# Optimization experiments

Hardware: AMD Instinct MI355X
Metric: run time of the kernel (lower is better)

Reference implementation:

```python
import jax, jax.numpy as jnp
import numpy as np

B, H, W, D = 16, 64, 64, 512

def setup_inputs() -> dict:
    key = jax.random.key(0)
    k1, k2, k3, k4, k5, k6 = jax.random.split(key, 6)
    x = jax.random.normal(k1, (B, H, W, D), dtype=jnp.float32)
    attentionXFull = jax.random.normal(k2, (B, H, W, W), dtype=jnp.float32)
    attentionYFull = jax.random.normal(k3, (B, W, H, H), dtype=jnp.float32)
    valueFull = jax.random.normal(k4, (B, H, W, D), dtype=jnp.float32)
    # Learned scalar Gaussian params: shift initialized positive, bias negative
    shift = jnp.abs(jax.random.normal(k5, (1,), dtype=jnp.float32))
    bias = -jnp.abs(jax.random.normal(k6, (1,), dtype=jnp.float32))
    return {"x": x, "attentionXFull": attentionXFull, "attentionYFull": attentionYFull,
            "valueFull": valueFull, "shift": shift, "bias": bias}

def reference(x, attentionXFull, attentionYFull, valueFull, shift, bias):
    # valueFull: [B,H,W,D]; attentionXFull: [B,H,W,W] (last axis = row positions h)
    # attentionYFull: [B,W,H,H] (indexed [b,c,r,w], last axis = col positions w)
    Bv, Hd, Wd, Dd = valueFull.shape
    cw = jnp.arange(Wd, dtype=valueFull.dtype)
    # disX[c,h] = -(shift*(h-c)^2 + bias)
    disX = -(shift[0] * (cw[None, :] - cw[:, None]) ** 2 + bias[0])  # [W,W]
    aX = jax.nn.sigmoid(disX[None, None, :, :] + attentionXFull)     # [B,H,W,W]
    outX = jnp.einsum('brch,brhd->brcd', aX, valueFull)              # row attention
    rh = jnp.arange(Hd, dtype=valueFull.dtype)
    # disY[r,w] = -(shift*(w-r)^2 + bias)
    disY = -(shift[0] * (rh[None, :] - rh[:, None]) ** 2 + bias[0])  # [H,H]
    aY = jax.nn.sigmoid(disY[None, None, :, :] + attentionYFull)     # [B,W,H,H] as [b,c,r,w]
    outY = jnp.einsum('bcrw,bwcd->brcd', aY, valueFull)              # column attention
    return outX + outY
```

## Files before the change

### kernel.cpp

```cpp
#include <hip/hip_runtime.h>
#include <stdint.h>


typedef __attribute__((ext_vector_type(8))) __bf16 bf16x8;
typedef __attribute__((ext_vector_type(8))) short short8;
typedef __attribute__((ext_vector_type(4))) float f32x4;
typedef __attribute__((ext_vector_type(4))) unsigned int uint4v;

union U8 { short8 s; bf16x8 b; unsigned short u[8]; uint4v q; };

__device__ __forceinline__ unsigned short f2bf(float f) {
    union { float f; unsigned int i; } v; v.f = f;
    return (unsigned short)((v.i + 0x7fffu + ((v.i >> 16) & 1u)) >> 16);
}
__device__ __forceinline__ float fsigmoid(float x) {
    float e = __builtin_amdgcn_exp2f(-1.44269504f * x);
    return __builtin_amdgcn_rcpf(1.0f + e);
}

template <int S_I, int S_K, bool ACCUM>
__global__ __launch_bounds__(256)
void gauss_gemm(const float* __restrict__ att,
                const float* __restrict__ V,
                float* __restrict__ out,
                const float* __restrict__ shiftp,
                const float* __restrict__ biasp) {
    __shared__ unsigned short S[4096];
    __shared__ unsigned short VT[128 * 66];

    const int bid    = blockIdx.x;
    const int dq     = bid & 3;
    const int i      = (bid >> 2) & 63;
    const int b      = bid >> 8;
    const int t      = threadIdx.x;
    const int dstart = dq * 128;

    const float shift = shiftp[0];
    const float bias  = biasp[0];

    const size_t base = (size_t)b * 2097152 + (size_t)i * S_I;

    const float* ab = att + (size_t)(b * 64 + i) * 4096;
#pragma unroll
    for (int chunk = 0; chunk < 2; ++chunk) {
        int flat = t + chunk * 256;
        int q = flat >> 6, m = flat & 63;
        const float* ap = ab + m * 64 + q * 8;
        f32x4 av0 = *(const f32x4*)(ap);
        f32x4 av1 = *(const f32x4*)(ap + 4);
        U8 res;
#pragma unroll
        for (int j = 0; j < 8; ++j) {
            float a    = (j < 4) ? av0[j & 3] : av1[j & 3];
            float diff = (float)(q * 8 + j - m);
            float dis  = -(shift * diff * diff + bias);
            res.u[j]   = f2bf(fsigmoid(dis + a));
        }
        *(short8*)(&S[flat * 8]) = res.s;
    }

    {
        const float* vb = V + base + dstart;
        const int d4 = t & 31;
        const int h0 = t >> 5;
#pragma unroll
        for (int it = 0; it < 8; ++it) {
            const int h = h0 + it * 8;
            f32x4 v = *(const f32x4*)(vb + (size_t)h * S_K + 4 * d4);
#pragma unroll
            for (int u = 0; u < 4; ++u)
                VT[(4 * d4 + u) * 66 + h] = f2bf(v[u]);
        }
    }
    __syncthreads();

    const int lane = t & 63, wid = t >> 6;
    const int l15 = lane & 15, quad = lane >> 4;

    f32x4 acc[4][2];
#pragma unroll
    for (int mt = 0; mt < 4; ++mt)
#pragma unroll
        for (int nt = 0; nt < 2; ++nt) acc[mt][nt] = (f32x4)0.0f;

#pragma unroll
    for (int ks = 0; ks < 2; ++ks) {
        bf16x8 af[4];
#pragma unroll
        for (int mt = 0; mt < 4; ++mt) {
            U8 a;
            a.s = *(const short8*)(&S[((ks * 4 + quad) * 64 + mt * 16 + l15) * 8]);
            af[mt] = a.b;
        }
        const int h = ks * 32 + quad * 8;
#pragma unroll
        for (int nt = 0; nt < 2; ++nt) {
            const int dloc = wid * 32 + nt * 16 + l15;
            const unsigned short* vp = &VT[dloc * 66 + h];
            U8 bvec;
            uint4v qv;
#pragma unroll
            for (int u = 0; u < 4; ++u) qv[u] = *(const unsigned int*)(vp + 2 * u);
            bvec.q = qv;
#pragma unroll
            for (int mt = 0; mt < 4; ++mt)
                acc[mt][nt] = __builtin_amdgcn_mfma_f32_16x16x32_bf16(
                    af[mt], bvec.b, acc[mt][nt], 0, 0, 0);
        }
    }

    float* ob = out + base + dstart;
#pragma unroll
    for (int mt = 0; mt < 4; ++mt)
#pragma unroll
        for (int nt = 0; nt < 2; ++nt)
#pragma unroll
            for (int reg = 0; reg < 4; ++reg) {
                int m = mt * 16 + quad * 4 + reg;
                int d = wid * 32 + nt * 16 + l15;
                size_t off = (size_t)m * S_K + d;
                float v = acc[mt][nt][reg];
                if (ACCUM) v += ob[off];
                ob[off] = v;
            }
}

extern "C" void kernel_launch(void* const* d_in, const int* in_sizes, int n_in,
                              void* d_out, int out_size, void* d_ws, size_t ws_size,
                              hipStream_t stream) {
    const float* attX = (const float*)d_in[1];
    const float* attY = (const float*)d_in[2];
    const float* V    = (const float*)d_in[3];
    const float* shp  = (const float*)d_in[4];
    const float* bip  = (const float*)d_in[5];
    float* out = (float*)d_out;

    dim3 blk(256);
    dim3 grid(16 * 64 * 4);
    gauss_gemm<32768, 512, false><<<grid, blk, 0, stream>>>(attX, V, out, shp, bip);
    gauss_gemm<512, 32768, true><<<grid, blk, 0, stream>>>(attY, V, out, shp, bip);
}
```

Measured before the change: 414.6 us.

## Precompute bf16 sigmoid attention and fuse row/column attention into one kernel

A new prep kernel computes the Gaussian-biased sigmoid for both attention tensors once and stores them as bf16 in the workspace. A fused kernel then computes row and column attention for a (batch, row-half, d-slice) tile. It keeps the row result in LDS as fp16 and adds it to the column result before a single write, which removes the output read-modify-write and the second pass over V. The risks are an extra round trip of the attention tensors through the workspace, fp16 rounding of the intermediate, and heavy LDS and register use. The old two-kernel path remains as a fallback when the workspace is too small.

```diff
diff --git a/kernel.cpp b/kernel.cpp
--- a/kernel.cpp
+++ b/kernel.cpp
@@ -6,6 +6,7 @@
 typedef __attribute__((ext_vector_type(8))) short short8;
 typedef __attribute__((ext_vector_type(4))) float f32x4;
 typedef __attribute__((ext_vector_type(4))) unsigned int uint4v;
+typedef __attribute__((ext_vector_type(4))) unsigned short u16x4;
 
 union U8 { short8 s; bf16x8 b; unsigned short u[8]; uint4v q; };
 
@@ -16,6 +17,192 @@
 __device__ __forceinline__ float fsigmoid(float x) {
     float e = __builtin_amdgcn_exp2f(-1.44269504f * x);
     return __builtin_amdgcn_rcpf(1.0f + e);
+}
+__device__ __forceinline__ unsigned short f2h(float f) {
+    union { _Float16 h; unsigned short u; } v; v.h = (_Float16)f; return v.u;
+}
+__device__ __forceinline__ float h2f(unsigned short u) {
+    union { _Float16 h; unsigned short us; } v; v.us = u; return (float)v.h;
+}
+
+__device__ __forceinline__ int sx_addr(int r, int d, int h) {
+    return r * 1024 + d * 64 + (h & 7) + ((((h >> 3) ^ (d & 7))) << 3);
+}
+__device__ __forceinline__ int sy_addr(int c, int d, int w) {
+    return c * 512 + d * 32 + (w & 7) + (((w >> 3) ^ (d & 3) ^ ((c & 1) << 1)) << 3);
+}
+__device__ __forceinline__ int ol_addr(int d, int r, int c) {
+    return d * 2048 + r * 64 + (c ^ ((r & 3) << 2) ^ ((d >> 2) << 4));
+}
+
+__device__ __forceinline__ void sig16(const float* __restrict__ in,
+                                      unsigned short* __restrict__ outp,
+                                      int l0, int sec, float shift, float bias) {
+    f32x4 v[4];
+#pragma unroll
+    for (int j = 0; j < 4; ++j) v[j] = *(const f32x4*)(in + 4 * j);
+    U8 r0, r1;
+#pragma unroll
+    for (int e = 0; e < 16; ++e) {
+        float dd = (float)(l0 + e - sec);
+        float dis = -(shift * dd * dd + bias);
+        unsigned short us = f2bf(fsigmoid(dis + v[e >> 2][e & 3]));
+        if (e < 8) r0.u[e] = us; else r1.u[e - 8] = us;
+    }
+    *(uint4v*)(outp) = r0.q;
+    *(uint4v*)(outp + 8) = r1.q;
+}
+
+__global__ __launch_bounds__(256)
+void prep_sig(const float* __restrict__ attX, const float* __restrict__ attY,
+              unsigned short* __restrict__ aX, unsigned short* __restrict__ aY,
+              const float* __restrict__ shiftp, const float* __restrict__ biasp) {
+    const float shift = shiftp[0];
+    const float bias  = biasp[0];
+    const size_t base = ((size_t)blockIdx.x * 256 + threadIdx.x) * 16;
+    const int sec = (int)((base >> 6) & 63);
+    const int l0  = (int)(base & 63);
+    sig16(attX + base, aX + base, l0, sec, shift, bias);
+    sig16(attY + base, aY + base, l0, sec, shift, bias);
+}
+
+__global__ __launch_bounds__(512, 2)
+void gauss_fused(const unsigned short* __restrict__ aX,
+                 const unsigned short* __restrict__ aY,
+                 const float* __restrict__ V,
+                 float* __restrict__ out) {
+    __shared__ unsigned short slab[32768];
+    __shared__ unsigned short olds[32768];
+
+    const int p   = blockIdx.x;
+    const int xcd = p & 7;
+    const int k   = p >> 3;
+    const int b   = ((k >> 5) << 3) | xcd;
+    const int dg  = (k & 31) >> 1;
+    const int rh  = k & 1;
+    const int rbase = rh * 32;
+
+    const int t    = threadIdx.x;
+    const int lane = t & 63;
+    const int wid  = t >> 6;
+    const int cg   = wid & 3;
+    const int rg   = wid >> 2;
+    const int l15  = lane & 15;
+    const int quad = lane >> 4;
+
+    const size_t vbase = (size_t)b * 2097152;
+
+#pragma unroll
+    for (int dc = 0; dc < 2; ++dc) {
+        const int dstart = dg * 32 + dc * 16;
+
+        __syncthreads();
+
+        {
+            const int r  = t >> 4;
+            const int hq = t & 15;
+            const float* vp = V + vbase + (size_t)(rbase + r) * 32768
+                            + (size_t)(4 * hq) * 512 + dstart;
+            f32x4 vv[4][4];
+#pragma unroll
+            for (int i = 0; i < 4; ++i)
+#pragma unroll
+                for (int j = 0; j < 4; ++j)
+                    vv[i][j] = *(const f32x4*)(vp + i * 512 + 4 * j);
+#pragma unroll
+            for (int d = 0; d < 16; ++d) {
+                u16x4 pk;
+#pragma unroll
+                for (int i = 0; i < 4; ++i) pk[i] = f2bf(vv[i][d >> 2][d & 3]);
+                *(u16x4*)&slab[sx_addr(r, d, 4 * hq)] = pk;
+            }
+        }
+        __syncthreads();
+
+        f32x4 accX[16];
+#pragma unroll
+        for (int rr = 0; rr < 16; ++rr) accX[rr] = (f32x4)0.0f;
+#pragma unroll
+        for (int ks = 0; ks < 2; ++ks) {
+            bf16x8 af[16];
+#pragma unroll
+            for (int rr = 0; rr < 16; ++rr) {
+                const unsigned short* ap = aX
+                    + ((size_t)((b * 64 + rbase + rg * 16 + rr) * 64 + (cg * 16 + l15))) * 64
+                    + ks * 32 + quad * 8;
+                U8 u; u.q = *(const uint4v*)ap; af[rr] = u.b;
+            }
+#pragma unroll
+            for (int rr = 0; rr < 16; ++rr) {
+                U8 bu;
+                bu.q = *(const uint4v*)&slab[sx_addr(rg * 16 + rr, l15, ks * 32 + quad * 8)];
+                accX[rr] = __builtin_amdgcn_mfma_f32_16x16x32_bf16(af[rr], bu.b, accX[rr], 0, 0, 0);
+            }
+        }
+
+#pragma unroll
+        for (int rr = 0; rr < 16; ++rr) {
+            u16x4 pk;
+#pragma unroll
+            for (int reg = 0; reg < 4; ++reg) pk[reg] = f2h(accX[rr][reg]);
+            *(u16x4*)&olds[ol_addr(l15, rg * 16 + rr, cg * 16 + quad * 4)] = pk;
+        }
+
+        f32x4 accY[16];
+#pragma unroll
+        for (int cc = 0; cc < 16; ++cc) accY[cc] = (f32x4)0.0f;
+#pragma unroll
+        for (int half = 0; half < 2; ++half) {
+            __syncthreads();
+            {
+                const int c  = t >> 3;
+                const int wq = t & 7;
+                const float* vp = V + vbase + (size_t)(half * 32 + 4 * wq) * 32768
+                                + (size_t)c * 512 + dstart;
+                f32x4 vv[4][4];
+#pragma unroll
+                for (int i = 0; i < 4; ++i)
+#pragma unroll
+                    for (int j = 0; j < 4; ++j)
+                        vv[i][j] = *(const f32x4*)(vp + (size_t)i * 32768 + 4 * j);
+#pragma unroll
+                for (int d = 0; d < 16; ++d) {
+                    u16x4 pk;
+#pragma unroll
+                    for (int i = 0; i < 4; ++i) pk[i] = f2bf(vv[i][d >> 2][d & 3]);
+                    *(u16x4*)&slab[sy_addr(c, d, 4 * wq)] = pk;
+                }
+            }
+            __syncthreads();
+            bf16x8 bg[16];
+#pragma unroll
+            for (int cc = 0; cc < 16; ++cc) {
+                const unsigned short* ap = aY
+                    + ((size_t)((b * 64 + cg * 16 + cc) * 64 + (rbase + rg * 16 + l15))) * 64
+                    + half * 32 + quad * 8;
+                U8 u; u.q = *(const uint4v*)ap; bg[cc] = u.b;
+            }
+#pragma unroll
+            for (int cc = 0; cc < 16; ++cc) {
+                U8 au;
+                au.q = *(const uint4v*)&slab[sy_addr(cg * 16 + cc, l15, quad * 8)];
+                accY[cc] = __builtin_amdgcn_mfma_f32_16x16x32_bf16(au.b, bg[cc], accY[cc], 0, 0, 0);
+            }
+        }
+
+        {
+            float* ob = out + vbase + (size_t)(rbase + rg * 16 + l15) * 32768 + dstart + quad * 4;
+#pragma unroll
+            for (int cc = 0; cc < 16; ++cc) {
+                f32x4 res;
+#pragma unroll
+                for (int reg = 0; reg < 4; ++reg)
+                    res[reg] = accY[cc][reg]
+                             + h2f(olds[ol_addr(quad * 4 + reg, rg * 16 + l15, cg * 16 + cc)]);
+                *(f32x4*)(ob + (size_t)(cg * 16 + cc) * 512) = res;
+            }
+        }
+    }
 }
 
 template <int S_I, int S_K, bool ACCUM>
@@ -37,7 +224,6 @@
 
     const float shift = shiftp[0];
     const float bias  = biasp[0];
-
     const size_t base = (size_t)b * 2097152 + (size_t)i * S_I;
 
     const float* ab = att + (size_t)(b * 64 + i) * 4096;
@@ -58,7 +244,6 @@
         }
         *(short8*)(&S[flat * 8]) = res.s;
     }
-
     {
         const float* vb = V + base + dstart;
         const int d4 = t & 31;
@@ -135,8 +320,16 @@
     const float* bip  = (const float*)d_in[5];
     float* out = (float*)d_out;
 
-    dim3 blk(256);
-    dim3 grid(16 * 64 * 4);
-    gauss_gemm<32768, 512, false><<<grid, blk, 0, stream>>>(attX, V, out, shp, bip);
-    gauss_gemm<512, 32768, true><<<grid, blk, 0, stream>>>(attY, V, out, shp, bip);
-}
+    const size_t ATT_ELEMS = 16ull * 64 * 64 * 64;
+    if (ws_size >= ATT_ELEMS * 2 * sizeof(unsigned short)) {
+        unsigned short* aXw = (unsigned short*)d_ws;
+        unsigned short* aYw = aXw + ATT_ELEMS;
+        prep_sig<<<dim3(1024), dim3(256), 0, stream>>>(attX, attY, aXw, aYw, shp, bip);
+        gauss_fused<<<dim3(512), dim3(512), 0, stream>>>(aXw, aYw, V, out);
+    } else {
+        dim3 blk(256);
+        dim3 grid(16 * 64 * 4);
+        gauss_gemm<32768, 512, false><<<grid, blk, 0, stream>>>(attX, V, out, shp, bip);
+        gauss_gemm<512, 32768, true><<<grid, blk, 0, stream>>>(attY, V, out, shp, bip);
+    }
+}
```

After: 474.8 us. 1.15x slower.

## Precompute bf16 sigmoid weights and retiled V, fuse row and column attention

Applied to the files above, without the earlier changes.

Adds a prep kernel that computes both Gaussian-biased sigmoid attention maps into bf16 workspace buffers. Two retile kernels also write transposed bf16 copies of V for the row and column directions. A single single-wave MFMA kernel then computes the row result, holds it in LDS as fp16, adds the column result and writes the output once. This removes the read-modify-write of the output between two passes. In exchange it adds extra workspace traffic for the retiled V copies and loses some precision by keeping the row partial in fp16. The old path is kept as a fallback when the workspace is too small.

```diff
diff --git a/kernel.cpp b/kernel.cpp
--- a/kernel.cpp
+++ b/kernel.cpp
@@ -6,6 +6,7 @@
 typedef __attribute__((ext_vector_type(8))) short short8;
 typedef __attribute__((ext_vector_type(4))) float f32x4;
 typedef __attribute__((ext_vector_type(4))) unsigned int uint4v;
+typedef __attribute__((ext_vector_type(4))) unsigned short u16x4;
 
 union U8 { short8 s; bf16x8 b; unsigned short u[8]; uint4v q; };
 
@@ -16,6 +17,142 @@
 __device__ __forceinline__ float fsigmoid(float x) {
     float e = __builtin_amdgcn_exp2f(-1.44269504f * x);
     return __builtin_amdgcn_rcpf(1.0f + e);
+}
+__device__ __forceinline__ unsigned short f2h(float f) {
+    union { _Float16 h; unsigned short u; } v; v.h = (_Float16)f; return v.u;
+}
+__device__ __forceinline__ float h2f(unsigned short u) {
+    union { _Float16 h; unsigned short us; } v; v.us = u; return (float)v.h;
+}
+
+__device__ __forceinline__ void sig16(const float* __restrict__ in,
+                                      unsigned short* __restrict__ outp,
+                                      int l0, int sec, float shift, float bias) {
+    f32x4 v[4];
+#pragma unroll
+    for (int j = 0; j < 4; ++j) v[j] = *(const f32x4*)(in + 4 * j);
+    U8 r0, r1;
+#pragma unroll
+    for (int e = 0; e < 16; ++e) {
+        float dd = (float)(l0 + e - sec);
+        float dis = -(shift * dd * dd + bias);
+        unsigned short us = f2bf(fsigmoid(dis + v[e >> 2][e & 3]));
+        if (e < 8) r0.u[e] = us; else r1.u[e - 8] = us;
+    }
+    *(uint4v*)(outp) = r0.q;
+    *(uint4v*)(outp + 8) = r1.q;
+}
+
+__global__ __launch_bounds__(256)
+void prep_sig(const float* __restrict__ attX, const float* __restrict__ attY,
+              unsigned short* __restrict__ aX, unsigned short* __restrict__ aY,
+              const float* __restrict__ shiftp, const float* __restrict__ biasp) {
+    const float shift = shiftp[0];
+    const float bias  = biasp[0];
+    const size_t base = ((size_t)blockIdx.x * 256 + threadIdx.x) * 16;
+    const int sec = (int)((base >> 6) & 63);
+    const int l0  = (int)(base & 63);
+    sig16(attX + base, aX + base, l0, sec, shift, bias);
+    sig16(attY + base, aY + base, l0, sec, shift, bias);
+}
+
+__global__ __launch_bounds__(256)
+void retile(const float* __restrict__ V, unsigned short* __restrict__ vt,
+            long long rowStride, long long strideB, long long strideI) {
+    __shared__ unsigned short T[64 * 72];
+    const int p = blockIdx.x;
+    const int t = threadIdx.x;
+    const float* src = V + (size_t)(p >> 6) * strideB + (size_t)(p & 63) * strideI;
+    unsigned short* dst = vt + (size_t)p * 32768;
+
+    for (int ch = 0; ch < 8; ++ch) {
+        const int j = t >> 2, qq = t & 3;
+        const float* sp = src + (size_t)j * rowStride + ch * 64 + qq * 16;
+        f32x4 x[4];
+#pragma unroll
+        for (int k = 0; k < 4; ++k) x[k] = *(const f32x4*)(sp + 4 * k);
+        if (ch) __syncthreads();
+        U8 w0, w1;
+#pragma unroll
+        for (int e = 0; e < 8; ++e) {
+            w0.u[e] = f2bf(x[e >> 2][e & 3]);
+            w1.u[e] = f2bf(x[2 + (e >> 2)][e & 3]);
+        }
+        *(uint4v*)(&T[j * 72 + qq * 16])     = w0.q;
+        *(uint4v*)(&T[j * 72 + qq * 16 + 8]) = w1.q;
+        __syncthreads();
+        const int d = t >> 2, part = t & 3;
+        U8 o0, o1;
+#pragma unroll
+        for (int jj = 0; jj < 8; ++jj) {
+            o0.u[jj] = T[(part * 16 + jj) * 72 + d];
+            o1.u[jj] = T[(part * 16 + 8 + jj) * 72 + d];
+        }
+        unsigned short* dp = dst + (size_t)(ch * 64 + d) * 64 + part * 16;
+        *(uint4v*)dp       = o0.q;
+        *(uint4v*)(dp + 8) = o1.q;
+    }
+}
+
+__global__ __launch_bounds__(64, 4)
+void gauss_mfma(const unsigned short* __restrict__ aX,
+                const unsigned short* __restrict__ aY,
+                const unsigned short* __restrict__ vtX,
+                const unsigned short* __restrict__ vtY,
+                float* __restrict__ out) {
+    __shared__ unsigned short olds[16 * 264 + 8];
+
+    const int p  = blockIdx.x;
+    const int b  = (p & 7) + (((p >> 3) >> 9) << 3);
+    const int q  = (p >> 3) & 511;
+    const int dt = q >> 4;
+    const int rt = (q >> 2) & 3;
+    const int ct = q & 3;
+
+    const int lane = threadIdx.x;
+    const int l15 = lane & 15, quad = lane >> 4;
+    const int dlo = dt * 16 + l15;
+
+#pragma unroll
+    for (int rr = 0; rr < 16; ++rr) {
+        const int r = rt * 16 + rr;
+        const unsigned short* vp = vtX + ((size_t)(b * 64 + r) * 512 + dlo) * 64 + quad * 8;
+        const unsigned short* ap = aX + ((size_t)(b * 64 + r) * 64 + ct * 16 + l15) * 64 + quad * 8;
+        U8 v0, v1, a0, a1;
+        v0.q = *(const uint4v*)vp;
+        v1.q = *(const uint4v*)(vp + 32);
+        a0.q = *(const uint4v*)ap;
+        a1.q = *(const uint4v*)(ap + 32);
+        f32x4 acc = (f32x4)0.0f;
+        acc = __builtin_amdgcn_mfma_f32_16x16x32_bf16(v0.b, a0.b, acc, 0, 0, 0);
+        acc = __builtin_amdgcn_mfma_f32_16x16x32_bf16(v1.b, a1.b, acc, 0, 0, 0);
+        u16x4 pk;
+#pragma unroll
+        for (int g = 0; g < 4; ++g) pk[g] = f2h(acc[g]);
+        *(u16x4*)&olds[rr * 264 + l15 * 16 + quad * 4] = pk;
+    }
+
+    float* ob = out + (size_t)b * 2097152 + (size_t)(rt * 16 + l15) * 32768
+              + (size_t)(ct * 16) * 512 + dt * 16 + quad * 4;
+#pragma unroll
+    for (int cc = 0; cc < 16; ++cc) {
+        const int c = ct * 16 + cc;
+        const unsigned short* wp = vtY + ((size_t)(b * 64 + c) * 512 + dlo) * 64 + quad * 8;
+        const unsigned short* bp = aY + ((size_t)(b * 64 + c) * 64 + rt * 16 + l15) * 64 + quad * 8;
+        U8 w0, w1, y0, y1;
+        w0.q = *(const uint4v*)wp;
+        w1.q = *(const uint4v*)(wp + 32);
+        y0.q = *(const uint4v*)bp;
+        y1.q = *(const uint4v*)(bp + 32);
+        f32x4 acc = (f32x4)0.0f;
+        acc = __builtin_amdgcn_mfma_f32_16x16x32_bf16(w0.b, y0.b, acc, 0, 0, 0);
+        acc = __builtin_amdgcn_mfma_f32_16x16x32_bf16(w1.b, y1.b, acc, 0, 0, 0);
+        u16x4 xp = *(const u16x4*)&olds[l15 * 264 + cc * 16 + quad * 4];
+        f32x4 res;
+#pragma unroll
+        for (int g = 0; g < 4; ++g) res[g] = acc[g] + h2f(xp[g]);
+        *(f32x4*)(ob + (size_t)cc * 512) = res;
+    }
 }
 
 template <int S_I, int S_K, bool ACCUM>
@@ -37,28 +174,26 @@
 
     const float shift = shiftp[0];
     const float bias  = biasp[0];
-
     const size_t base = (size_t)b * 2097152 + (size_t)i * S_I;
 
     const float* ab = att + (size_t)(b * 64 + i) * 4096;
 #pragma unroll
     for (int chunk = 0; chunk < 2; ++chunk) {
         int flat = t + chunk * 256;
-        int q = flat >> 6, m = flat & 63;
-        const float* ap = ab + m * 64 + q * 8;
+        int qd = flat >> 6, m = flat & 63;
+        const float* ap = ab + m * 64 + qd * 8;
         f32x4 av0 = *(const f32x4*)(ap);
         f32x4 av1 = *(const f32x4*)(ap + 4);
         U8 res;
 #pragma unroll
         for (int j = 0; j < 8; ++j) {
             float a    = (j < 4) ? av0[j & 3] : av1[j & 3];
-            float diff = (float)(q * 8 + j - m);
+            float diff = (float)(qd * 8 + j - m);
             float dis  = -(shift * diff * diff + bias);
             res.u[j]   = f2bf(fsigmoid(dis + a));
         }
         *(short8*)(&S[flat * 8]) = res.s;
     }
-
     {
         const float* vb = V + base + dstart;
         const int d4 = t & 31;
@@ -135,8 +270,23 @@
     const float* bip  = (const float*)d_in[5];
     float* out = (float*)d_out;
 
-    dim3 blk(256);
-    dim3 grid(16 * 64 * 4);
-    gauss_gemm<32768, 512, false><<<grid, blk, 0, stream>>>(attX, V, out, shp, bip);
-    gauss_gemm<512, 32768, true><<<grid, blk, 0, stream>>>(attY, V, out, shp, bip);
-}
+    const size_t A_ELEMS  = 4194304;
+    const size_t VT_ELEMS = 33554432;
+    const size_t NEED = (2 * A_ELEMS + 2 * VT_ELEMS) * sizeof(unsigned short);
+
+    if (ws_size >= NEED) {
+        unsigned short* aXw = (unsigned short*)d_ws;
+        unsigned short* aYw = aXw + A_ELEMS;
+        unsigned short* vtX = aYw + A_ELEMS;
+        unsigned short* vtY = vtX + VT_ELEMS;
+        prep_sig<<<dim3(1024), dim3(256), 0, stream>>>(attX, attY, aXw, aYw, shp, bip);
+        retile<<<dim3(1024), dim3(256), 0, stream>>>(V, vtX, 512LL, 2097152LL, 32768LL);
+        retile<<<dim3(1024), dim3(256), 0, stream>>>(V, vtY, 32768LL, 2097152LL, 512LL);
+        gauss_mfma<<<dim3(8192), dim3(64), 0, stream>>>(aXw, aYw, vtX, vtY, out);
+    } else {
+        dim3 blk(256);
+        dim3 grid(16 * 64 * 4);
+        gauss_gemm<32768, 512, false><<<grid, blk, 0, stream>>>(attX, V, out, shp, bip);
+        gauss_gemm<512, 32768, true><<<grid, blk, 0, stream>>>(attY, V, out, shp, bip);
+    }
+}
```

Result: slower. 492.5 us (+18.8%).

## Precompute bf16 sigmoid gates and fuse row and column attention into one kernel

Applied to the files above, without the earlier changes.

A prep kernel computes the Gaussian-biased sigmoid gates for both attention tensors once and stores them as bf16 in workspace. A new fused kernel computes the row-attention result for a 16x16 spatial tile, parks it in shared memory as fp16, then computes the column attention for the same tile and writes the sum once. This removes the read-modify-write of the output between two kernels and the repeated sigmoid evaluation per d-quarter. In exchange, V is gathered with strided scalar loads, without a shared-memory transpose, and the row-attention partial is rounded to fp16 before the final add. The old two-kernel path stays as a fallback when the workspace is too small.

```diff
diff --git a/kernel.cpp b/kernel.cpp
--- a/kernel.cpp
+++ b/kernel.cpp
@@ -6,6 +6,7 @@
 typedef __attribute__((ext_vector_type(8))) short short8;
 typedef __attribute__((ext_vector_type(4))) float f32x4;
 typedef __attribute__((ext_vector_type(4))) unsigned int uint4v;
+typedef __attribute__((ext_vector_type(4))) unsigned short u16x4;
 
 union U8 { short8 s; bf16x8 b; unsigned short u[8]; uint4v q; };
 
@@ -16,6 +17,127 @@
 __device__ __forceinline__ float fsigmoid(float x) {
     float e = __builtin_amdgcn_exp2f(-1.44269504f * x);
     return __builtin_amdgcn_rcpf(1.0f + e);
+}
+__device__ __forceinline__ unsigned short f2h(float f) {
+    union { _Float16 h; unsigned short u; } v; v.h = (_Float16)f; return v.u;
+}
+__device__ __forceinline__ float h2f(unsigned short u) {
+    union { _Float16 h; unsigned short us; } v; v.us = u; return (float)v.h;
+}
+
+__device__ __forceinline__ void sig16(const float* __restrict__ in,
+                                      unsigned short* __restrict__ outp,
+                                      int l0, int sec, float shift, float bias) {
+    f32x4 v[4];
+#pragma unroll
+    for (int j = 0; j < 4; ++j) v[j] = *(const f32x4*)(in + 4 * j);
+    U8 r0, r1;
+#pragma unroll
+    for (int e = 0; e < 16; ++e) {
+        float dd = (float)(l0 + e - sec);
+        float dis = -(shift * dd * dd + bias);
+        unsigned short us = f2bf(fsigmoid(dis + v[e >> 2][e & 3]));
+        if (e < 8) r0.u[e] = us; else r1.u[e - 8] = us;
+    }
+    *(uint4v*)(outp) = r0.q;
+    *(uint4v*)(outp + 8) = r1.q;
+}
+
+__global__ __launch_bounds__(256)
+void prep_sig(const float* __restrict__ attX, const float* __restrict__ attY,
+              unsigned short* __restrict__ aX, unsigned short* __restrict__ aY,
+              const float* __restrict__ shiftp, const float* __restrict__ biasp) {
+    const float shift = shiftp[0];
+    const float bias  = biasp[0];
+    const size_t base = ((size_t)blockIdx.x * 256 + threadIdx.x) * 16;
+    const int sec = (int)((base >> 6) & 63);
+    const int l0  = (int)(base & 63);
+    sig16(attX + base, aX + base, l0, sec, shift, bias);
+    sig16(attY + base, aY + base, l0, sec, shift, bias);
+}
+
+__global__ __launch_bounds__(256, 4)
+void gauss_fused2(const unsigned short* __restrict__ aX,
+                  const unsigned short* __restrict__ aY,
+                  const float* __restrict__ V,
+                  float* __restrict__ out) {
+    __shared__ unsigned short park[4 * 4224];
+
+    const int p   = blockIdx.x;
+    const int xcd = p & 7;
+    const int s   = p >> 3;
+    const int b   = xcd + ((s >> 6) << 3);
+    const int rem = s & 63;
+    const int dt  = rem >> 2;
+    const int rt  = rem & 3;
+
+    const int t    = threadIdx.x;
+    const int lane = t & 63;
+    const int ct   = t >> 6;
+    const int l15  = lane & 15, quad = lane >> 4;
+
+    unsigned short* pk = &park[ct * 4224];
+
+    const size_t vbase = (size_t)b * 2097152;
+    const unsigned short* aXb = aX + (size_t)b * 262144;
+    const unsigned short* aYb = aY + (size_t)b * 262144;
+
+    for (int dc = 0; dc < 2; ++dc) {
+        const int dcol = dt * 32 + dc * 16 + l15;
+
+        const float* vxw = V + vbase + (size_t)(rt * 16) * 32768 + dcol;
+        const unsigned short* axw = aXb + ((size_t)(rt * 16) * 64 + ct * 16 + l15) * 64 + quad * 8;
+#pragma unroll 2
+        for (int rr = 0; rr < 16; ++rr) {
+            const float* vp = vxw + (size_t)rr * 32768;
+            const unsigned short* ap = axw + (size_t)rr * 4096;
+            f32x4 acc = (f32x4)0.0f;
+#pragma unroll
+            for (int ks = 0; ks < 2; ++ks) {
+                const int h0 = ks * 32 + quad * 8;
+                float vf[8];
+#pragma unroll
+                for (int j = 0; j < 8; ++j) vf[j] = vp[(h0 + j) * 512];
+                U8 a; a.q = *(const uint4v*)(ap + ks * 32);
+                U8 bb;
+#pragma unroll
+                for (int j = 0; j < 8; ++j) bb.u[j] = f2bf(vf[j]);
+                acc = __builtin_amdgcn_mfma_f32_16x16x32_bf16(a.b, bb.b, acc, 0, 0, 0);
+            }
+            u16x4 w;
+#pragma unroll
+            for (int g = 0; g < 4; ++g) w[g] = f2h(acc[g]);
+            *(u16x4*)&pk[l15 * 264 + rr * 16 + quad * 4] = w;
+        }
+
+        const float* vyw = V + vbase + (size_t)(ct * 16) * 512 + dcol;
+        const unsigned short* ayw = aYb + ((size_t)(ct * 16) * 64 + rt * 16 + l15) * 64 + quad * 8;
+        float* ow = out + vbase + (size_t)(rt * 16 + quad * 4) * 32768
+                  + (size_t)(ct * 16) * 512 + dcol;
+#pragma unroll 2
+        for (int cc = 0; cc < 16; ++cc) {
+            const float* vp = vyw + (size_t)cc * 512;
+            const unsigned short* ap = ayw + (size_t)cc * 4096;
+            f32x4 acc = (f32x4)0.0f;
+#pragma unroll
+            for (int ks = 0; ks < 2; ++ks) {
+                const int w0 = ks * 32 + quad * 8;
+                float vf[8];
+#pragma unroll
+                for (int j = 0; j < 8; ++j) vf[j] = vp[(size_t)(w0 + j) * 32768];
+                U8 a; a.q = *(const uint4v*)(ap + ks * 32);
+                U8 bb;
+#pragma unroll
+                for (int j = 0; j < 8; ++j) bb.u[j] = f2bf(vf[j]);
+                acc = __builtin_amdgcn_mfma_f32_16x16x32_bf16(a.b, bb.b, acc, 0, 0, 0);
+            }
+#pragma unroll
+            for (int g = 0; g < 4; ++g) {
+                float xv = h2f(pk[l15 * 264 + (quad * 4 + g) * 16 + cc]);
+                ow[(size_t)g * 32768 + (size_t)cc * 512] = acc[g] + xv;
+            }
+        }
+    }
 }
 
 template <int S_I, int S_K, bool ACCUM>
@@ -37,28 +159,26 @@
 
     const float shift = shiftp[0];
     const float bias  = biasp[0];
-
     const size_t base = (size_t)b * 2097152 + (size_t)i * S_I;
 
     const float* ab = att + (size_t)(b * 64 + i) * 4096;
 #pragma unroll
     for (int chunk = 0; chunk < 2; ++chunk) {
         int flat = t + chunk * 256;
-        int q = flat >> 6, m = flat & 63;
-        const float* ap = ab + m * 64 + q * 8;
+        int qd = flat >> 6, m = flat & 63;
+        const float* ap = ab + m * 64 + qd * 8;
         f32x4 av0 = *(const f32x4*)(ap);
         f32x4 av1 = *(const f32x4*)(ap + 4);
         U8 res;
 #pragma unroll
         for (int j = 0; j < 8; ++j) {
             float a    = (j < 4) ? av0[j & 3] : av1[j & 3];
-            float diff = (float)(q * 8 + j - m);
+            float diff = (float)(qd * 8 + j - m);
             float dis  = -(shift * diff * diff + bias);
             res.u[j]   = f2bf(fsigmoid(dis + a));
         }
         *(short8*)(&S[flat * 8]) = res.s;
     }
-
     {
         const float* vb = V + base + dstart;
         const int d4 = t & 31;
@@ -135,8 +255,18 @@
     const float* bip  = (const float*)d_in[5];
     float* out = (float*)d_out;
 
-    dim3 blk(256);
-    dim3 grid(16 * 64 * 4);
-    gauss_gemm<32768, 512, false><<<grid, blk, 0, stream>>>(attX, V, out, shp, bip);
-    gauss_gemm<512, 32768, true><<<grid, blk, 0, stream>>>(attY, V, out, shp, bip);
-}
+    const size_t A_ELEMS = 4194304;
+    const size_t NEED = 2 * A_ELEMS * sizeof(unsigned short);
+
+    if (ws_size >= NEED) {
+        unsigned short* aXw = (unsigned short*)d_ws;
+        unsigned short* aYw = aXw + A_ELEMS;
+        prep_sig<<<dim3(1024), dim3(256), 0, stream>>>(attX, attY, aXw, aYw, shp, bip);
+        gauss_fused2<<<dim3(1024), dim3(256), 0, stream>>>(aXw, aYw, V, out);
+    } else {
+        dim3 blk(256);
+        dim3 grid(16 * 64 * 4);
+        gauss_gemm<32768, 512, false><<<grid, blk, 0, stream>>>(attX, V, out, shp, bip);
+        gauss_gemm<512, 32768, true><<<grid, blk, 0, stream>>>(attY, V, out, shp, bip);
+    }
+}
```

New measurement: 465.6 us. 1.12x slower.
